# Kernel tuning notes

Measured on AMD Instinct MI355X. Metric: run time of the kernel, lower is better.

The kernel has to match this reference:

```python
import jax, jax.numpy as jnp
import numpy as np

B, N, D, H = 2, 2048, 1024, 16
HD = D // H


def precompute_freqs_cis(dim, end, theta=10000.0):
    freqs = 1.0 / theta ** (jnp.arange(0, dim, 2)[: dim // 2].astype(jnp.float32) / dim)
    t = jnp.arange(end, dtype=jnp.float32)
    freqs = jnp.outer(t, freqs)  # [N, dim//2]
    return jax.lax.complex(jnp.cos(freqs), jnp.sin(freqs))


def apply_rotary(q, k, freqs_cis):
    # q,k: [B,H,N,HD]; freqs_cis: [N, HD//2] broadcasts over B,H
    qr = q.reshape(q.shape[:-1] + (-1, 2))
    kr = k.reshape(k.shape[:-1] + (-1, 2))
    qc = jax.lax.complex(qr[..., 0], qr[..., 1]) * freqs_cis
    kc = jax.lax.complex(kr[..., 0], kr[..., 1]) * freqs_cis
    q_out = jnp.stack([jnp.real(qc), jnp.imag(qc)], axis=-1).reshape(q.shape)
    k_out = jnp.stack([jnp.real(kc), jnp.imag(kc)], axis=-1).reshape(k.shape)
    return q_out, k_out


def setup_inputs() -> dict:
    key = jax.random.key(0)
    ks = jax.random.split(key, 5)
    s = 1.0 / np.sqrt(D)
    return {
        "x": jax.random.normal(ks[0], (B, N, D), dtype=jnp.float32),
        "Wq": jax.random.normal(ks[1], (D, D), dtype=jnp.float32) * s,
        "Wk": jax.random.normal(ks[2], (D, D), dtype=jnp.float32) * s,
        "Wv": jax.random.normal(ks[3], (D, D), dtype=jnp.float32) * s,
        "Wo": jax.random.normal(ks[4], (D, D), dtype=jnp.float32) * s,
    }


def reference(x, Wq, Wk, Wv, Wo):
    b, n, d = x.shape
    h, hd = H, d // H
    q = (x @ Wq).reshape(b, n, h, hd).transpose(0, 2, 1, 3)
    k = (x @ Wk).reshape(b, n, h, hd).transpose(0, 2, 1, 3)
    v = (x @ Wv).reshape(b, n, h, hd).transpose(0, 2, 1, 3)
    freqs_cis = precompute_freqs_cis(hd, n)
    q, k = apply_rotary(q, k, freqs_cis)
    scale = hd ** (-0.5)
    attn = jnp.einsum("bhqd,bhkd->bhqk", q, k) * scale
    attn = jax.nn.softmax(attn, axis=-1)
    out = jnp.einsum("bhqk,bhkd->bhqd", attn, v)
    out = out.transpose(0, 2, 1, 3).reshape(b, n, d)
    return out @ Wo
```

## Files before the change

### kernel.cpp

```cpp
#include <hip/hip_runtime.h>

typedef unsigned short u16;
typedef short  bf16x8 __attribute__((ext_vector_type(8)));
typedef u16    u16x8  __attribute__((ext_vector_type(8)));
typedef float  f32x4  __attribute__((ext_vector_type(4)));
typedef float  f32x2  __attribute__((ext_vector_type(2)));
typedef int    i32x4  __attribute__((ext_vector_type(4)));
typedef unsigned u32x4 __attribute__((ext_vector_type(4)));

__device__ __forceinline__ u16 f2bf(float f) {
  union { float f; unsigned u; } x; x.f = f;
  return (u16)((x.u + 0x7fffu + ((x.u >> 16) & 1u)) >> 16);
}

__device__ __forceinline__ unsigned pk2bf(float a, float b) {
  unsigned r;
  asm("v_cvt_pk_bf16_f32 %0, %1, %2" : "=v"(r) : "v"(a), "v"(b));
  return r;
}

__device__ __forceinline__ float exp2v(float x) {
  float r;
  asm("v_exp_f32 %0, %1" : "=v"(r) : "v"(x));
  return r;
}

__device__ __forceinline__ void gload16(const void* g, void* lds) {
  __builtin_amdgcn_global_load_lds((const __attribute__((address_space(1))) unsigned int*)g,
                                   (__attribute__((address_space(3))) unsigned int*)lds,
                                   16, 0, 0);
}

__device__ __forceinline__ bf16x8 lds8(const u16* base, int row, int colb) {
  int off = (row << 7) + colb;
  off ^= (row & 7) << 4;
  return *(const bf16x8*)((const char*)base + off);
}

__device__ __forceinline__ bf16x8 lds32(const u16* base, int row, int lg) {
  int off = (row << 6) + ((lg ^ (row & 3)) << 4);
  return *(const bf16x8*)((const char*)base + off);
}


__global__ __launch_bounds__(256) void cast_x_k(const float* __restrict__ x,
                                                u16* __restrict__ xb) {
  int i = (blockIdx.x * 256 + threadIdx.x) * 8;
  float4 a = *(const float4*)&x[i];
  float4 b = *(const float4*)&x[i + 4];
  u16x8 o;
  o[0] = f2bf(a.x); o[1] = f2bf(a.y); o[2] = f2bf(a.z); o[3] = f2bf(a.w);
  o[4] = f2bf(b.x); o[5] = f2bf(b.y); o[6] = f2bf(b.z); o[7] = f2bf(b.w);
  *(u16x8*)&xb[i] = o;
}

__global__ __launch_bounds__(256) void transpose_cast_k(const float* __restrict__ Wq,
                                                        const float* __restrict__ Wk,
                                                        const float* __restrict__ Wv,
                                                        const float* __restrict__ Wo,
                                                        u16* __restrict__ WqkvT,
                                                        u16* __restrict__ WoT) {
  __shared__ u16 tile[64][72];
  int z = blockIdx.z;
  const float* W = (z == 0) ? Wq : (z == 1) ? Wk : (z == 2) ? Wv : Wo;
  u16* dst = (z < 3) ? (WqkvT + z * 1024 * 1024) : WoT;
  int k0 = blockIdx.y << 6, nn0 = blockIdx.x << 6;
  int t = threadIdx.x;
#pragma unroll
  for (int p = 0; p < 4; ++p) {
    int kr = (p << 4) + (t >> 4), c4 = (t & 15) << 2;
    float4 v = *(const float4*)&W[(k0 + kr) * 1024 + nn0 + c4];
    tile[c4 + 0][kr] = f2bf(v.x); tile[c4 + 1][kr] = f2bf(v.y);
    tile[c4 + 2][kr] = f2bf(v.z); tile[c4 + 3][kr] = f2bf(v.w);
  }
  __syncthreads();
#pragma unroll
  for (int p = 0; p < 2; ++p) {
    int nr = (p << 5) + (t >> 3), c8 = (t & 7) << 3;
    i32x4 vv = *(const i32x4*)&tile[nr][c8];
    *(i32x4*)&dst[(nn0 + nr) * 1024 + k0 + c8] = vv;
  }
}

__global__ __launch_bounds__(256) void rope_table_k(f32x2* __restrict__ ctab) {
  int idx = blockIdx.x * 256 + threadIdx.x;
  int i = idx & 31, p = idx >> 5;
  float freq = powf(10000.0f, -(float)(2 * i) * (1.0f / 64.0f));
  float ang = (float)p * freq;
  f32x2 v; v[0] = cosf(ang); v[1] = sinf(ang);
  ctab[idx] = v;
}


__global__ __launch_bounds__(256) void gemm_qkv_k(const u16* __restrict__ A,
                                                  const u16* __restrict__ BT,
                                                  u16* __restrict__ Qb,
                                                  u16* __restrict__ Kb,
                                                  u16* __restrict__ VbT,
                                                  const f32x2* __restrict__ ctab) {
  __shared__ u16 As[3][128 * 32];
  __shared__ u16 Bs[3][128 * 32];
  const int K = 1024;
  const int m0 = blockIdx.y << 7, n0 = blockIdx.x << 7;
  const int t = threadIdx.x, w = t >> 6, l = t & 63;
  const int wr = (w >> 1) << 6, wc = (w & 1) << 6;
  const int lr = l & 15, lg = l >> 4;
  const int g_row = l >> 2;
  const int g_col = (((l & 3) ^ ((l >> 2) & 3)) << 3);

  auto stage = [&](int buf, int kt) {
    const int k0_ = kt << 5;
#pragma unroll
    for (int it = 0; it < 2; ++it) {
      int seg = (w << 1) + it;
      int row = (seg << 4) + g_row;
      gload16(&A[(m0 + row) * K + k0_ + g_col], (char*)As[buf] + seg * 1024);
      gload16(&BT[(n0 + row) * K + k0_ + g_col], (char*)Bs[buf] + seg * 1024);
    }
  };

  f32x4 acc[4][4] = {};

  stage(0, 0);
  stage(1, 1);

#pragma unroll
  for (int kt = 0; kt < 32; ++kt) {
    if (kt < 31) asm volatile("s_waitcnt vmcnt(4)" ::: "memory");
    else         asm volatile("s_waitcnt vmcnt(0)" ::: "memory");
    __builtin_amdgcn_s_barrier();
    __builtin_amdgcn_sched_barrier(0);
    if (kt < 30) stage((kt + 2) % 3, kt + 2);
    const u16* Ab = As[kt % 3];
    const u16* Bb = Bs[kt % 3];
    bf16x8 af[4], bfr[4];
#pragma unroll
    for (int m = 0; m < 4; ++m) af[m] = lds32(Ab, wr + (m << 4) + lr, lg);
#pragma unroll
    for (int n = 0; n < 4; ++n) bfr[n] = lds32(Bb, wc + (n << 4) + lr, lg);
#pragma unroll
    for (int m = 0; m < 4; ++m)
#pragma unroll
      for (int n = 0; n < 4; ++n)
        acc[m][n] = __builtin_amdgcn_mfma_f32_16x16x32_bf16(af[m], bfr[n], acc[m][n], 0, 0, 0);
  }

  const int region = n0 >> 10;
  if (region < 2) {
    const float qscale = 0.125f * 1.44269504088896f;
#pragma unroll
    for (int m = 0; m < 4; ++m)
#pragma unroll
      for (int n = 0; n < 4; ++n) {
        const int col = n0 + wc + (n << 4) + lr;
        const int hd = col & 63;
#pragma unroll
        for (int r = 0; r < 4; ++r) {
          const int row = m0 + wr + (m << 4) + (lg << 2) + r;
          float v = acc[m][n][r];
          float p = __shfl_xor(v, 1);
          f32x2 cs = ctab[(row & 2047) * 32 + (hd >> 1)];
          float o = (hd & 1) ? (p * cs[1] + v * cs[0]) : (v * cs[0] - p * cs[1]);
          if (region == 0) { o *= qscale; Qb[row * 1024 + (col & 1023)] = f2bf(o); }
          else             { Kb[row * 1024 + (col & 1023)] = f2bf(o); }
        }
      }
  } else {
#pragma unroll
    for (int m = 0; m < 4; ++m)
#pragma unroll
      for (int n = 0; n < 4; ++n) {
        const int cv = n0 + wc + (n << 4) + lr - 2048;
        const int hh = cv >> 6, dim = cv & 63;
#pragma unroll
        for (int r = 0; r < 4; ++r) {
          const int row = m0 + wr + (m << 4) + (lg << 2) + r;
          const int bb = row >> 11, pos = row & 2047;
          const int k6 = pos & 63;
          const int pp = (k6 & 3) | (((k6 >> 4) & 1) << 2) | (((k6 >> 2) & 3) << 3)
                       | (((k6 >> 5) & 1) << 5);
          const int posp = (pos & ~63) | pp;
          VbT[(((bb << 4) + hh) << 6 | dim) * 2048 + posp] = f2bf(acc[m][n][r]);
        }
      }
  }
}


__global__ __launch_bounds__(256) void gemm_out_k(const u16* __restrict__ A,
                                                  const u16* __restrict__ BT,
                                                  float* __restrict__ C) {
  __shared__ u16 As[3][64 * 32];
  __shared__ u16 Bs[3][128 * 32];
  const int K = 1024;
  const int m0 = blockIdx.y << 6, n0 = blockIdx.x << 7;
  const int t = threadIdx.x, w = t >> 6, l = t & 63;
  const int wr = (w & 1) << 5, wc = (w >> 1) << 6;
  const int lr = l & 15, lg = l >> 4;
  const int g_row = l >> 2;
  const int g_col = (((l & 3) ^ ((l >> 2) & 3)) << 3);

  auto stage = [&](int buf, int kt) {
    const int k0_ = kt << 5;
    {
      int rowA = (w << 4) + g_row;
      gload16(&A[(m0 + rowA) * K + k0_ + g_col], (char*)As[buf] + w * 1024);
    }
#pragma unroll
    for (int it = 0; it < 2; ++it) {
      int seg = (w << 1) + it;
      int row = (seg << 4) + g_row;
      gload16(&BT[(n0 + row) * K + k0_ + g_col], (char*)Bs[buf] + seg * 1024);
    }
  };

  f32x4 acc[2][4] = {};

  stage(0, 0);
  stage(1, 1);

#pragma unroll
  for (int kt = 0; kt < 32; ++kt) {
    if (kt < 31) asm volatile("s_waitcnt vmcnt(3)" ::: "memory");
    else         asm volatile("s_waitcnt vmcnt(0)" ::: "memory");
    __builtin_amdgcn_s_barrier();
    __builtin_amdgcn_sched_barrier(0);
    if (kt < 30) stage((kt + 2) % 3, kt + 2);
    const u16* Ab = As[kt % 3];
    const u16* Bb = Bs[kt % 3];
    bf16x8 af[2], bfr[4];
#pragma unroll
    for (int m = 0; m < 2; ++m) af[m] = lds32(Ab, wr + (m << 4) + lr, lg);
#pragma unroll
    for (int n = 0; n < 4; ++n) bfr[n] = lds32(Bb, wc + (n << 4) + lr, lg);
#pragma unroll
    for (int m = 0; m < 2; ++m)
#pragma unroll
      for (int n = 0; n < 4; ++n)
        acc[m][n] = __builtin_amdgcn_mfma_f32_16x16x32_bf16(af[m], bfr[n], acc[m][n], 0, 0, 0);
  }

#pragma unroll
  for (int m = 0; m < 2; ++m)
#pragma unroll
    for (int n = 0; n < 4; ++n) {
      const int col = n0 + wc + (n << 4) + lr;
#pragma unroll
      for (int r = 0; r < 4; ++r) {
        const int row = m0 + wr + (m << 4) + (lg << 2) + r;
        C[row * 1024 + col] = acc[m][n][r];
      }
    }
}


__global__ __launch_bounds__(256) void attn_k(const u16* __restrict__ Qb,
                                              const u16* __restrict__ Kb,
                                              const u16* __restrict__ VbT,
                                              u16* __restrict__ Ob) {
  __shared__ u16 Ks[2][2][64 * 64];
  __shared__ u16 Vs[2][2][64 * 64];

  const int lin = blockIdx.x;
  const int xcd = lin & 7, rest = lin >> 3;
  const int bh = (xcd << 2) + (rest & 3);
  const int qt = rest >> 2;
  const int b = bh >> 4;
  const int t = threadIdx.x, w = t >> 6, l = t & 63;
  const int lr = l & 15, lg = l >> 4;
  const int rb = b << 11;
  const int cb = (bh & 15) << 6;
  const int srow = l >> 3;
  const int scol = ((l & 7) ^ srow) << 3;

  auto kv_stage = [&](int buf, int st) {
#pragma unroll
    for (int sub = 0; sub < 2; ++sub) {
      const int tile = (st << 1) + sub;
#pragma unroll
      for (int it = 0; it < 2; ++it) {
        int seg = (w << 1) + it;
        int row = (seg << 3) + srow;
        gload16(&Kb[(size_t)(rb + (tile << 6) + row) * 1024 + cb + scol],
                (char*)Ks[buf][sub] + seg * 1024);
        gload16(&VbT[(size_t)((bh << 6) + row) * 2048 + (tile << 6) + scol],
                (char*)Vs[buf][sub] + seg * 1024);
      }
    }
  };

  bf16x8 qf[2][2];
#pragma unroll
  for (int g = 0; g < 2; ++g)
#pragma unroll
    for (int kk = 0; kk < 2; ++kk)
      qf[g][kk] = *(const bf16x8*)&Qb[(size_t)(rb + (qt << 7) + (w << 5) + (g << 4) + lr) * 1024
                                      + cb + (kk << 5) + (lg << 3)];

  kv_stage(0, 0);
  asm volatile("s_waitcnt vmcnt(0)" ::: "memory");
  __builtin_amdgcn_s_barrier();
  __builtin_amdgcn_sched_barrier(0);

  const f32x4 z4 = {0.f, 0.f, 0.f, 0.f};
  float lsum[2] = {0.f, 0.f};
  f32x4 Oacc[2][4] = {};

  for (int st = 0; st < 16; ++st) {
    const int buf = st & 1;
    if (st < 15) kv_stage(buf ^ 1, st + 1);

#pragma unroll
    for (int sub = 0; sub < 2; ++sub) {
      const u16* Kc = Ks[buf][sub];
      const u16* Vc = Vs[buf][sub];

      unsigned U[2][4][2];
#pragma unroll
      for (int c = 0; c < 4; ++c) {
        bf16x8 kf0 = lds8(Kc, (c << 4) + lr, (lg << 4));
        bf16x8 kf1 = lds8(Kc, (c << 4) + lr, 64 + (lg << 4));
        f32x4 S[2];
        __builtin_amdgcn_s_setprio(1);
#pragma unroll
        for (int g = 0; g < 2; ++g) {
          S[g] = __builtin_amdgcn_mfma_f32_16x16x32_bf16(kf0, qf[g][0], z4, 0, 0, 0);
          S[g] = __builtin_amdgcn_mfma_f32_16x16x32_bf16(kf1, qf[g][1], S[g], 0, 0, 0);
        }
        __builtin_amdgcn_s_setprio(0);
#pragma unroll
        for (int g = 0; g < 2; ++g) {
          float q0 = exp2v(S[g][0]), q1 = exp2v(S[g][1]);
          float q2 = exp2v(S[g][2]), q3 = exp2v(S[g][3]);
          lsum[g] += (q0 + q1) + (q2 + q3);
          U[g][c][0] = pk2bf(q0, q1);
          U[g][c][1] = pk2bf(q2, q3);
        }
      }

#pragma unroll
      for (int kk2 = 0; kk2 < 2; ++kk2) {
        bf16x8 vf[4];
#pragma unroll
        for (int df = 0; df < 4; ++df)
          vf[df] = lds8(Vc, (df << 4) + lr, (kk2 << 6) + (lg << 4));
        __builtin_amdgcn_s_setprio(1);
#pragma unroll
        for (int g = 0; g < 2; ++g) {
          u32x4 pt;
          pt[0] = U[g][2 * kk2][0];     pt[1] = U[g][2 * kk2][1];
          pt[2] = U[g][2 * kk2 + 1][0]; pt[3] = U[g][2 * kk2 + 1][1];
          bf16x8 pa = *(const bf16x8*)&pt;
#pragma unroll
          for (int df = 0; df < 4; ++df)
            Oacc[g][df] = __builtin_amdgcn_mfma_f32_16x16x32_bf16(pa, vf[df], Oacc[g][df], 0, 0, 0);
        }
        __builtin_amdgcn_s_setprio(0);
      }
    }

    asm volatile("s_waitcnt vmcnt(0)" ::: "memory");
    __builtin_amdgcn_s_barrier();
    __builtin_amdgcn_sched_barrier(0);
  }

#pragma unroll
  for (int g = 0; g < 2; ++g) {
    float ls = lsum[g];
    ls += __shfl_xor(ls, 16);
    ls += __shfl_xor(ls, 32);
    float lq[4];
#pragma unroll
    for (int r = 0; r < 4; ++r) lq[r] = 1.f / __shfl(ls, (lg << 2) + r);
#pragma unroll
    for (int df = 0; df < 4; ++df)
#pragma unroll
      for (int r = 0; r < 4; ++r) {
        int row = (qt << 7) + (w << 5) + (g << 4) + (lg << 2) + r;
        int col = (df << 4) + lr;
        Ob[(size_t)(rb + row) * 1024 + cb + col] = f2bf(Oacc[g][df][r] * lq[r]);
      }
  }
}


extern "C" void kernel_launch(void* const* d_in, const int* in_sizes, int n_in,
                              void* d_out, int out_size, void* d_ws, size_t ws_size,
                              hipStream_t stream) {
  const float* x  = (const float*)d_in[0];
  const float* Wq = (const float*)d_in[1];
  const float* Wk = (const float*)d_in[2];
  const float* Wv = (const float*)d_in[3];
  const float* Wo = (const float*)d_in[4];
  float* out = (float*)d_out;

  char* ws = (char*)d_ws;
  u16* xb     = (u16*)(ws);
  u16* WqkvT  = (u16*)(ws + 8388608);
  u16* WoT    = (u16*)(ws + 14680064);
  u16* Qb     = (u16*)(ws + 16777216);
  u16* Kb     = (u16*)(ws + 25165824);
  u16* VbT    = (u16*)(ws + 33554432);
  f32x2* ctab = (f32x2*)(ws + 41943040);
  u16* Ob = xb;

  cast_x_k<<<2048, 256, 0, stream>>>(x, xb);
  dim3 gt(16, 16, 4);
  transpose_cast_k<<<gt, 256, 0, stream>>>(Wq, Wk, Wv, Wo, WqkvT, WoT);
  rope_table_k<<<256, 256, 0, stream>>>(ctab);

  dim3 gq(24, 32);
  gemm_qkv_k<<<gq, 256, 0, stream>>>(xb, WqkvT, Qb, Kb, VbT, ctab);

  attn_k<<<512, 256, 0, stream>>>(Qb, Kb, VbT, Ob);

  dim3 go(8, 64);
  gemm_out_k<<<go, 256, 0, stream>>>(Ob, WoT, out);
}
```

Baseline: 120.6 us.

## Enlarge QKV GEMM tile to 256x256 with 512 threads and XCD-aware block mapping

The QKV projection GEMM moves from 128x128 tiles with 256 threads to 256x256 tiles with 512 threads, and each wave now computes 128x64. The launch becomes a 1D grid of 192 blocks, remapped so that each XCD gets two adjacent row bands, which should improve L2 reuse. The larger tile raises arithmetic intensity per loaded byte. In exchange, LDS use grows to 96KB, there are fewer blocks than CUs (192 vs 256), and register pressure is higher with 32 accumulators per lane.

New measurement: 132.0 us. 9.4% more time.

```diff
diff --git a/kernel.cpp b/kernel.cpp
--- a/kernel.cpp
+++ b/kernel.cpp
@@ -92,64 +92,71 @@
 }
 
 
-__global__ __launch_bounds__(256) void gemm_qkv_k(const u16* __restrict__ A,
+__global__ __launch_bounds__(512) void gemm_qkv_k(const u16* __restrict__ A,
                                                   const u16* __restrict__ BT,
                                                   u16* __restrict__ Qb,
                                                   u16* __restrict__ Kb,
                                                   u16* __restrict__ VbT,
                                                   const f32x2* __restrict__ ctab) {
-  __shared__ u16 As[3][128 * 32];
-  __shared__ u16 Bs[3][128 * 32];
+  __shared__ u16 As[3][256 * 32];
+  __shared__ u16 Bs[3][256 * 32];
   const int K = 1024;
-  const int m0 = blockIdx.y << 7, n0 = blockIdx.x << 7;
+  const int lin = blockIdx.x;
+  const int xcd = lin & 7, idx = lin >> 3;
+  const int by = (xcd << 1) + (idx >= 12 ? 1 : 0);
+  const int bx = (idx >= 12) ? (idx - 12) : idx;
+  const int m0 = by << 8, n0 = bx << 8;
   const int t = threadIdx.x, w = t >> 6, l = t & 63;
-  const int wr = (w >> 1) << 6, wc = (w & 1) << 6;
+  const int wm = w >> 2, wn = w & 3;
+  const int wr = wm << 7, wc = wn << 6;
   const int lr = l & 15, lg = l >> 4;
   const int g_row = l >> 2;
   const int g_col = (((l & 3) ^ ((l >> 2) & 3)) << 3);
 
-  auto stage = [&](int buf, int kt) {
+  auto stage = [&](u16* ab, u16* bb, int kt) {
     const int k0_ = kt << 5;
 #pragma unroll
     for (int it = 0; it < 2; ++it) {
       int seg = (w << 1) + it;
       int row = (seg << 4) + g_row;
-      gload16(&A[(m0 + row) * K + k0_ + g_col], (char*)As[buf] + seg * 1024);
-      gload16(&BT[(n0 + row) * K + k0_ + g_col], (char*)Bs[buf] + seg * 1024);
+      gload16(&A[(m0 + row) * K + k0_ + g_col], (char*)ab + seg * 1024);
+      gload16(&BT[(n0 + row) * K + k0_ + g_col], (char*)bb + seg * 1024);
     }
   };
 
-  f32x4 acc[4][4] = {};
-
-  stage(0, 0);
-  stage(1, 1);
-
-#pragma unroll
+  f32x4 acc[8][4] = {};
+
+  u16 *a0 = As[0], *a1 = As[1], *a2 = As[2];
+  u16 *b0 = Bs[0], *b1 = Bs[1], *b2 = Bs[2];
+
+  stage(a0, b0, 0);
+  stage(a1, b1, 1);
+
   for (int kt = 0; kt < 32; ++kt) {
     if (kt < 31) asm volatile("s_waitcnt vmcnt(4)" ::: "memory");
     else         asm volatile("s_waitcnt vmcnt(0)" ::: "memory");
     __builtin_amdgcn_s_barrier();
     __builtin_amdgcn_sched_barrier(0);
-    if (kt < 30) stage((kt + 2) % 3, kt + 2);
-    const u16* Ab = As[kt % 3];
-    const u16* Bb = Bs[kt % 3];
-    bf16x8 af[4], bfr[4];
-#pragma unroll
-    for (int m = 0; m < 4; ++m) af[m] = lds32(Ab, wr + (m << 4) + lr, lg);
-#pragma unroll
-    for (int n = 0; n < 4; ++n) bfr[n] = lds32(Bb, wc + (n << 4) + lr, lg);
-#pragma unroll
-    for (int m = 0; m < 4; ++m)
+    if (kt < 30) stage(a2, b2, kt + 2);
+    bf16x8 af[8], bfr[4];
+#pragma unroll
+    for (int m = 0; m < 8; ++m) af[m] = lds32(a0, wr + (m << 4) + lr, lg);
+#pragma unroll
+    for (int n = 0; n < 4; ++n) bfr[n] = lds32(b0, wc + (n << 4) + lr, lg);
+#pragma unroll
+    for (int m = 0; m < 8; ++m)
 #pragma unroll
       for (int n = 0; n < 4; ++n)
         acc[m][n] = __builtin_amdgcn_mfma_f32_16x16x32_bf16(af[m], bfr[n], acc[m][n], 0, 0, 0);
+    u16* tp = a0; a0 = a1; a1 = a2; a2 = tp;
+    tp = b0; b0 = b1; b1 = b2; b2 = tp;
   }
 
   const int region = n0 >> 10;
   if (region < 2) {
     const float qscale = 0.125f * 1.44269504088896f;
 #pragma unroll
-    for (int m = 0; m < 4; ++m)
+    for (int m = 0; m < 8; ++m)
 #pragma unroll
       for (int n = 0; n < 4; ++n) {
         const int col = n0 + wc + (n << 4) + lr;
@@ -167,7 +174,7 @@
       }
   } else {
 #pragma unroll
-    for (int m = 0; m < 4; ++m)
+    for (int m = 0; m < 8; ++m)
 #pragma unroll
       for (int n = 0; n < 4; ++n) {
         const int cv = n0 + wc + (n << 4) + lr - 2048;
@@ -409,8 +416,7 @@
   transpose_cast_k<<<gt, 256, 0, stream>>>(Wq, Wk, Wv, Wo, WqkvT, WoT);
   rope_table_k<<<256, 256, 0, stream>>>(ctab);
 
-  dim3 gq(24, 32);
-  gemm_qkv_k<<<gq, 256, 0, stream>>>(xb, WqkvT, Qb, Kb, VbT, ctab);
+  gemm_qkv_k<<<192, 512, 0, stream>>>(xb, WqkvT, Qb, Kb, VbT, ctab);
 
   attn_k<<<512, 256, 0, stream>>>(Qb, Kb, VbT, Ob);
 
```

## Halve attention block size to 64 queries and add MFMA priority in GEMMs

Applied to the files above, without the earlier changes.

The attention kernel now runs 1024 blocks of 128 threads, each handling 64 query rows, and stages one 64-key K/V tile per iteration instead of two. This raises the block count and cuts LDS per block, so more blocks can be resident across CUs, at the cost of each K/V tile being loaded by twice as many blocks and of more barriers per key. The two GEMM kernels also wrap their MFMA inner loops in s_setprio so the matrix work is issued ahead of other waves.

Result: slower. 124.2 us (+3.0%).

```diff
diff --git a/kernel.cpp b/kernel.cpp
--- a/kernel.cpp
+++ b/kernel.cpp
@@ -138,11 +138,13 @@
     for (int m = 0; m < 4; ++m) af[m] = lds32(Ab, wr + (m << 4) + lr, lg);
 #pragma unroll
     for (int n = 0; n < 4; ++n) bfr[n] = lds32(Bb, wc + (n << 4) + lr, lg);
+    __builtin_amdgcn_s_setprio(1);
 #pragma unroll
     for (int m = 0; m < 4; ++m)
 #pragma unroll
       for (int n = 0; n < 4; ++n)
         acc[m][n] = __builtin_amdgcn_mfma_f32_16x16x32_bf16(af[m], bfr[n], acc[m][n], 0, 0, 0);
+    __builtin_amdgcn_s_setprio(0);
   }
 
   const int region = n0 >> 10;
@@ -233,11 +235,13 @@
     for (int m = 0; m < 2; ++m) af[m] = lds32(Ab, wr + (m << 4) + lr, lg);
 #pragma unroll
     for (int n = 0; n < 4; ++n) bfr[n] = lds32(Bb, wc + (n << 4) + lr, lg);
+    __builtin_amdgcn_s_setprio(1);
 #pragma unroll
     for (int m = 0; m < 2; ++m)
 #pragma unroll
       for (int n = 0; n < 4; ++n)
         acc[m][n] = __builtin_amdgcn_mfma_f32_16x16x32_bf16(af[m], bfr[n], acc[m][n], 0, 0, 0);
+    __builtin_amdgcn_s_setprio(0);
   }
 
 #pragma unroll
@@ -254,12 +258,12 @@
 }
 
 
-__global__ __launch_bounds__(256) void attn_k(const u16* __restrict__ Qb,
+__global__ __launch_bounds__(128) void attn_k(const u16* __restrict__ Qb,
                                               const u16* __restrict__ Kb,
                                               const u16* __restrict__ VbT,
                                               u16* __restrict__ Ob) {
-  __shared__ u16 Ks[2][2][64 * 64];
-  __shared__ u16 Vs[2][2][64 * 64];
+  __shared__ u16 Ks[2][64 * 64];
+  __shared__ u16 Vs[2][64 * 64];
 
   const int lin = blockIdx.x;
   const int xcd = lin & 7, rest = lin >> 3;
@@ -273,19 +277,15 @@
   const int srow = l >> 3;
   const int scol = ((l & 7) ^ srow) << 3;
 
-  auto kv_stage = [&](int buf, int st) {
-#pragma unroll
-    for (int sub = 0; sub < 2; ++sub) {
-      const int tile = (st << 1) + sub;
-#pragma unroll
-      for (int it = 0; it < 2; ++it) {
-        int seg = (w << 1) + it;
-        int row = (seg << 3) + srow;
-        gload16(&Kb[(size_t)(rb + (tile << 6) + row) * 1024 + cb + scol],
-                (char*)Ks[buf][sub] + seg * 1024);
-        gload16(&VbT[(size_t)((bh << 6) + row) * 2048 + (tile << 6) + scol],
-                (char*)Vs[buf][sub] + seg * 1024);
-      }
+  auto kv_stage = [&](int buf, int tile) {
+#pragma unroll
+    for (int it = 0; it < 4; ++it) {
+      int seg = (w << 2) + it;
+      int row = (seg << 3) + srow;
+      gload16(&Kb[(size_t)(rb + (tile << 6) + row) * 1024 + cb + scol],
+              (char*)Ks[buf] + seg * 1024);
+      gload16(&VbT[(size_t)((bh << 6) + row) * 2048 + (tile << 6) + scol],
+              (char*)Vs[buf] + seg * 1024);
     }
   };
 
@@ -294,7 +294,7 @@
   for (int g = 0; g < 2; ++g)
 #pragma unroll
     for (int kk = 0; kk < 2; ++kk)
-      qf[g][kk] = *(const bf16x8*)&Qb[(size_t)(rb + (qt << 7) + (w << 5) + (g << 4) + lr) * 1024
+      qf[g][kk] = *(const bf16x8*)&Qb[(size_t)(rb + (qt << 6) + (w << 5) + (g << 4) + lr) * 1024
                                       + cb + (kk << 5) + (lg << 3)];
 
   kv_stage(0, 0);
@@ -306,57 +306,54 @@
   float lsum[2] = {0.f, 0.f};
   f32x4 Oacc[2][4] = {};
 
-  for (int st = 0; st < 16; ++st) {
-    const int buf = st & 1;
-    if (st < 15) kv_stage(buf ^ 1, st + 1);
-
-#pragma unroll
-    for (int sub = 0; sub < 2; ++sub) {
-      const u16* Kc = Ks[buf][sub];
-      const u16* Vc = Vs[buf][sub];
-
-      unsigned U[2][4][2];
-#pragma unroll
-      for (int c = 0; c < 4; ++c) {
-        bf16x8 kf0 = lds8(Kc, (c << 4) + lr, (lg << 4));
-        bf16x8 kf1 = lds8(Kc, (c << 4) + lr, 64 + (lg << 4));
-        f32x4 S[2];
-        __builtin_amdgcn_s_setprio(1);
-#pragma unroll
-        for (int g = 0; g < 2; ++g) {
-          S[g] = __builtin_amdgcn_mfma_f32_16x16x32_bf16(kf0, qf[g][0], z4, 0, 0, 0);
-          S[g] = __builtin_amdgcn_mfma_f32_16x16x32_bf16(kf1, qf[g][1], S[g], 0, 0, 0);
-        }
-        __builtin_amdgcn_s_setprio(0);
-#pragma unroll
-        for (int g = 0; g < 2; ++g) {
-          float q0 = exp2v(S[g][0]), q1 = exp2v(S[g][1]);
-          float q2 = exp2v(S[g][2]), q3 = exp2v(S[g][3]);
-          lsum[g] += (q0 + q1) + (q2 + q3);
-          U[g][c][0] = pk2bf(q0, q1);
-          U[g][c][1] = pk2bf(q2, q3);
-        }
-      }
-
-#pragma unroll
-      for (int kk2 = 0; kk2 < 2; ++kk2) {
-        bf16x8 vf[4];
+  for (int kt = 0; kt < 32; ++kt) {
+    const int buf = kt & 1;
+    if (kt < 31) kv_stage(buf ^ 1, kt + 1);
+
+    const u16* Kc = Ks[buf];
+    const u16* Vc = Vs[buf];
+
+    unsigned U[2][4][2];
+#pragma unroll
+    for (int c = 0; c < 4; ++c) {
+      bf16x8 kf0 = lds8(Kc, (c << 4) + lr, (lg << 4));
+      bf16x8 kf1 = lds8(Kc, (c << 4) + lr, 64 + (lg << 4));
+      f32x4 S[2];
+      __builtin_amdgcn_s_setprio(1);
+#pragma unroll
+      for (int g = 0; g < 2; ++g) {
+        S[g] = __builtin_amdgcn_mfma_f32_16x16x32_bf16(kf0, qf[g][0], z4, 0, 0, 0);
+        S[g] = __builtin_amdgcn_mfma_f32_16x16x32_bf16(kf1, qf[g][1], S[g], 0, 0, 0);
+      }
+      __builtin_amdgcn_s_setprio(0);
+#pragma unroll
+      for (int g = 0; g < 2; ++g) {
+        float q0 = exp2v(S[g][0]), q1 = exp2v(S[g][1]);
+        float q2 = exp2v(S[g][2]), q3 = exp2v(S[g][3]);
+        lsum[g] += (q0 + q1) + (q2 + q3);
+        U[g][c][0] = pk2bf(q0, q1);
+        U[g][c][1] = pk2bf(q2, q3);
+      }
+    }
+
+#pragma unroll
+    for (int kk2 = 0; kk2 < 2; ++kk2) {
+      bf16x8 vf[4];
+#pragma unroll
+      for (int df = 0; df < 4; ++df)
+        vf[df] = lds8(Vc, (df << 4) + lr, (kk2 << 6) + (lg << 4));
+      __builtin_amdgcn_s_setprio(1);
+#pragma unroll
+      for (int g = 0; g < 2; ++g) {
+        u32x4 pt;
+        pt[0] = U[g][2 * kk2][0];     pt[1] = U[g][2 * kk2][1];
+        pt[2] = U[g][2 * kk2 + 1][0]; pt[3] = U[g][2 * kk2 + 1][1];
+        bf16x8 pa = *(const bf16x8*)&pt;
 #pragma unroll
         for (int df = 0; df < 4; ++df)
-          vf[df] = lds8(Vc, (df << 4) + lr, (kk2 << 6) + (lg << 4));
-        __builtin_amdgcn_s_setprio(1);
-#pragma unroll
-        for (int g = 0; g < 2; ++g) {
-          u32x4 pt;
-          pt[0] = U[g][2 * kk2][0];     pt[1] = U[g][2 * kk2][1];
-          pt[2] = U[g][2 * kk2 + 1][0]; pt[3] = U[g][2 * kk2 + 1][1];
-          bf16x8 pa = *(const bf16x8*)&pt;
-#pragma unroll
-          for (int df = 0; df < 4; ++df)
-            Oacc[g][df] = __builtin_amdgcn_mfma_f32_16x16x32_bf16(pa, vf[df], Oacc[g][df], 0, 0, 0);
-        }
-        __builtin_amdgcn_s_setprio(0);
-      }
+          Oacc[g][df] = __builtin_amdgcn_mfma_f32_16x16x32_bf16(pa, vf[df], Oacc[g][df], 0, 0, 0);
+      }
+      __builtin_amdgcn_s_setprio(0);
     }
 
     asm volatile("s_waitcnt vmcnt(0)" ::: "memory");
@@ -376,7 +373,7 @@
     for (int df = 0; df < 4; ++df)
 #pragma unroll
       for (int r = 0; r < 4; ++r) {
-        int row = (qt << 7) + (w << 5) + (g << 4) + (lg << 2) + r;
+        int row = (qt << 6) + (w << 5) + (g << 4) + (lg << 2) + r;
         int col = (df << 4) + lr;
         Ob[(size_t)(rb + row) * 1024 + cb + col] = f2bf(Oacc[g][df][r] * lq[r]);
       }
@@ -412,7 +409,7 @@
   dim3 gq(24, 32);
   gemm_qkv_k<<<gq, 256, 0, stream>>>(xb, WqkvT, Qb, Kb, VbT, ctab);
 
-  attn_k<<<512, 256, 0, stream>>>(Qb, Kb, VbT, Ob);
+  attn_k<<<1024, 128, 0, stream>>>(Qb, Kb, VbT, Ob);
 
   dim3 go(8, 64);
   gemm_out_k<<<go, 256, 0, stream>>>(Ob, WoT, out);
```

## Merge prep kernels into one launch and compute softmax row sums via MFMA

Applied to the files above, without the earlier changes.

Three preprocessing kernels (x cast, weight transpose-cast, rope table) are merged into a single launch with block-index dispatch, saving two kernel launches and their gaps. In attention, the per-lane scalar row-sum accumulation of exp values is replaced by an extra MFMA of P against a ones vector. This moves the sum onto the matrix unit and removes the final shuffle reduction. The trade-offs are one extra MFMA per P tile, and the sum is now taken over bf16-rounded probabilities, which matches the numerator more closely.

Result: faster. 113.3 us (-6.0%).

```diff
diff --git a/kernel.cpp b/kernel.cpp
--- a/kernel.cpp
+++ b/kernel.cpp
@@ -43,52 +43,55 @@
 }
 
 
-__global__ __launch_bounds__(256) void cast_x_k(const float* __restrict__ x,
-                                                u16* __restrict__ xb) {
-  int i = (blockIdx.x * 256 + threadIdx.x) * 8;
-  float4 a = *(const float4*)&x[i];
-  float4 b = *(const float4*)&x[i + 4];
-  u16x8 o;
-  o[0] = f2bf(a.x); o[1] = f2bf(a.y); o[2] = f2bf(a.z); o[3] = f2bf(a.w);
-  o[4] = f2bf(b.x); o[5] = f2bf(b.y); o[6] = f2bf(b.z); o[7] = f2bf(b.w);
-  *(u16x8*)&xb[i] = o;
-}
-
-__global__ __launch_bounds__(256) void transpose_cast_k(const float* __restrict__ Wq,
-                                                        const float* __restrict__ Wk,
-                                                        const float* __restrict__ Wv,
-                                                        const float* __restrict__ Wo,
-                                                        u16* __restrict__ WqkvT,
-                                                        u16* __restrict__ WoT) {
+__global__ __launch_bounds__(256) void prep_k(const float* __restrict__ x,
+                                              const float* __restrict__ Wq,
+                                              const float* __restrict__ Wk,
+                                              const float* __restrict__ Wv,
+                                              const float* __restrict__ Wo,
+                                              u16* __restrict__ xb,
+                                              u16* __restrict__ WqkvT,
+                                              u16* __restrict__ WoT,
+                                              f32x2* __restrict__ ctab) {
   __shared__ u16 tile[64][72];
-  int z = blockIdx.z;
-  const float* W = (z == 0) ? Wq : (z == 1) ? Wk : (z == 2) ? Wv : Wo;
-  u16* dst = (z < 3) ? (WqkvT + z * 1024 * 1024) : WoT;
-  int k0 = blockIdx.y << 6, nn0 = blockIdx.x << 6;
-  int t = threadIdx.x;
-#pragma unroll
-  for (int p = 0; p < 4; ++p) {
-    int kr = (p << 4) + (t >> 4), c4 = (t & 15) << 2;
-    float4 v = *(const float4*)&W[(k0 + kr) * 1024 + nn0 + c4];
-    tile[c4 + 0][kr] = f2bf(v.x); tile[c4 + 1][kr] = f2bf(v.y);
-    tile[c4 + 2][kr] = f2bf(v.z); tile[c4 + 3][kr] = f2bf(v.w);
-  }
-  __syncthreads();
-#pragma unroll
-  for (int p = 0; p < 2; ++p) {
-    int nr = (p << 5) + (t >> 3), c8 = (t & 7) << 3;
-    i32x4 vv = *(const i32x4*)&tile[nr][c8];
-    *(i32x4*)&dst[(nn0 + nr) * 1024 + k0 + c8] = vv;
-  }
-}
-
-__global__ __launch_bounds__(256) void rope_table_k(f32x2* __restrict__ ctab) {
-  int idx = blockIdx.x * 256 + threadIdx.x;
-  int i = idx & 31, p = idx >> 5;
-  float freq = powf(10000.0f, -(float)(2 * i) * (1.0f / 64.0f));
-  float ang = (float)p * freq;
-  f32x2 v; v[0] = cosf(ang); v[1] = sinf(ang);
-  ctab[idx] = v;
+  const int bid = blockIdx.x;
+  const int t = threadIdx.x;
+
+  if (bid < 2048) {
+    int i = (bid * 256 + t) * 8;
+    float4 a = *(const float4*)&x[i];
+    float4 b = *(const float4*)&x[i + 4];
+    u16x8 o;
+    o[0] = f2bf(a.x); o[1] = f2bf(a.y); o[2] = f2bf(a.z); o[3] = f2bf(a.w);
+    o[4] = f2bf(b.x); o[5] = f2bf(b.y); o[6] = f2bf(b.z); o[7] = f2bf(b.w);
+    *(u16x8*)&xb[i] = o;
+  } else if (bid < 3072) {
+    int b2 = bid - 2048;
+    int z = b2 >> 8, rem = b2 & 255;
+    int k0 = (rem >> 4) << 6, nn0 = (rem & 15) << 6;
+    const float* W = (z == 0) ? Wq : (z == 1) ? Wk : (z == 2) ? Wv : Wo;
+    u16* dst = (z < 3) ? (WqkvT + z * 1024 * 1024) : WoT;
+#pragma unroll
+    for (int p = 0; p < 4; ++p) {
+      int kr = (p << 4) + (t >> 4), c4 = (t & 15) << 2;
+      float4 v = *(const float4*)&W[(k0 + kr) * 1024 + nn0 + c4];
+      tile[c4 + 0][kr] = f2bf(v.x); tile[c4 + 1][kr] = f2bf(v.y);
+      tile[c4 + 2][kr] = f2bf(v.z); tile[c4 + 3][kr] = f2bf(v.w);
+    }
+    __syncthreads();
+#pragma unroll
+    for (int p = 0; p < 2; ++p) {
+      int nr = (p << 5) + (t >> 3), c8 = (t & 7) << 3;
+      i32x4 vv = *(const i32x4*)&tile[nr][c8];
+      *(i32x4*)&dst[(nn0 + nr) * 1024 + k0 + c8] = vv;
+    }
+  } else {
+    int idx = (bid - 3072) * 256 + t;
+    int i = idx & 31, p = idx >> 5;
+    float freq = powf(10000.0f, -(float)(2 * i) * (1.0f / 64.0f));
+    float ang = (float)p * freq;
+    f32x2 v; v[0] = cosf(ang); v[1] = sinf(ang);
+    ctab[idx] = v;
+  }
 }
 
 
@@ -297,13 +300,19 @@
       qf[g][kk] = *(const bf16x8*)&Qb[(size_t)(rb + (qt << 7) + (w << 5) + (g << 4) + lr) * 1024
                                       + cb + (kk << 5) + (lg << 3)];
 
+  bf16x8 vones;
+  {
+    u32x4 to; to[0] = 0x3F803F80u; to[1] = 0x3F803F80u; to[2] = 0x3F803F80u; to[3] = 0x3F803F80u;
+    vones = *(const bf16x8*)&to;
+  }
+
   kv_stage(0, 0);
   asm volatile("s_waitcnt vmcnt(0)" ::: "memory");
   __builtin_amdgcn_s_barrier();
   __builtin_amdgcn_sched_barrier(0);
 
   const f32x4 z4 = {0.f, 0.f, 0.f, 0.f};
-  float lsum[2] = {0.f, 0.f};
+  f32x4 Osum[2] = {};
   f32x4 Oacc[2][4] = {};
 
   for (int st = 0; st < 16; ++st) {
@@ -332,7 +341,6 @@
         for (int g = 0; g < 2; ++g) {
           float q0 = exp2v(S[g][0]), q1 = exp2v(S[g][1]);
           float q2 = exp2v(S[g][2]), q3 = exp2v(S[g][3]);
-          lsum[g] += (q0 + q1) + (q2 + q3);
           U[g][c][0] = pk2bf(q0, q1);
           U[g][c][1] = pk2bf(q2, q3);
         }
@@ -354,6 +362,7 @@
 #pragma unroll
           for (int df = 0; df < 4; ++df)
             Oacc[g][df] = __builtin_amdgcn_mfma_f32_16x16x32_bf16(pa, vf[df], Oacc[g][df], 0, 0, 0);
+          Osum[g] = __builtin_amdgcn_mfma_f32_16x16x32_bf16(pa, vones, Osum[g], 0, 0, 0);
         }
         __builtin_amdgcn_s_setprio(0);
       }
@@ -366,12 +375,9 @@
 
 #pragma unroll
   for (int g = 0; g < 2; ++g) {
-    float ls = lsum[g];
-    ls += __shfl_xor(ls, 16);
-    ls += __shfl_xor(ls, 32);
     float lq[4];
 #pragma unroll
-    for (int r = 0; r < 4; ++r) lq[r] = 1.f / __shfl(ls, (lg << 2) + r);
+    for (int r = 0; r < 4; ++r) lq[r] = 1.f / Osum[g][r];
 #pragma unroll
     for (int df = 0; df < 4; ++df)
 #pragma unroll
@@ -404,10 +410,7 @@
   f32x2* ctab = (f32x2*)(ws + 41943040);
   u16* Ob = xb;
 
-  cast_x_k<<<2048, 256, 0, stream>>>(x, xb);
-  dim3 gt(16, 16, 4);
-  transpose_cast_k<<<gt, 256, 0, stream>>>(Wq, Wk, Wv, Wo, WqkvT, WoT);
-  rope_table_k<<<256, 256, 0, stream>>>(ctab);
+  prep_k<<<3328, 256, 0, stream>>>(x, Wq, Wk, Wv, Wo, xb, WqkvT, WoT, ctab);
 
   dim3 gq(24, 32);
   gemm_qkv_k<<<gq, 256, 0, stream>>>(xb, WqkvT, Qb, Kb, VbT, ctab);
```
